# Optimization experiments

Measured on AMD Instinct MI355X. Metric: run time of the kernel, lower is better.

Reference implementation:

```python
import jax, jax.numpy as jnp
import numpy as np

NUM_HEADS = 16
CLAMP = 1e4


def setup_inputs() -> dict:
    key = jax.random.key(0)
    ks = jax.random.split(key, 8)
    B, Nq, Nkv, Cq, Ckv = 4, 2048, 2048, 1024, 768
    s_q = 1.0 / np.sqrt(Cq)
    s_kv = 1.0 / np.sqrt(Ckv)
    return {
        "query": jax.random.normal(ks[0], (B, Nq, Cq), jnp.float32),
        "key_value": jax.random.normal(ks[1], (B, Nkv, Ckv), jnp.float32),
        "Wq": jax.random.normal(ks[2], (Cq, Cq), jnp.float32) * s_q,
        "bq": jnp.zeros((Cq,), jnp.float32),
        "Wk": jax.random.normal(ks[3], (Ckv, Cq), jnp.float32) * s_kv,
        "bk": jnp.zeros((Cq,), jnp.float32),
        "Wv": jax.random.normal(ks[4], (Ckv, Cq), jnp.float32) * s_kv,
        "bv": jnp.zeros((Cq,), jnp.float32),
        "Wo": jax.random.normal(ks[5], (Cq, Cq), jnp.float32) * s_q,
        "bo": jnp.zeros((Cq,), jnp.float32),
    }


def reference(query, key_value, Wq, bq, Wk, bk, Wv, bv, Wo, bo):
    B, Nq, Cq = query.shape
    Nkv = key_value.shape[1]
    H = NUM_HEADS
    D = Cq // H
    scale = D ** (-0.5)

    # projections -> [B, H, N, D]
    q = (query @ Wq + bq).reshape(B, Nq, H, D).transpose(0, 2, 1, 3)
    k = (key_value @ Wk + bk).reshape(B, Nkv, H, D).transpose(0, 2, 1, 3)
    v = (key_value @ Wv + bv).reshape(B, Nkv, H, D).transpose(0, 2, 1, 3)

    # scores [B, H, Nq, Nkv] with clamp (mask=None path)
    attn = jnp.einsum("bhqd,bhkd->bhqk", q, k) * scale
    attn = jnp.clip(attn, -CLAMP, CLAMP)
    attn = jax.nn.softmax(attn, axis=-1)
    # NaN fallback: replace with uniform attention if any NaN present
    attn = jnp.where(jnp.any(jnp.isnan(attn)),
                     jnp.asarray(1.0 / Nkv, attn.dtype), attn)

    # weighted sum -> [B, Nq, Cq]
    x = jnp.einsum("bhqk,bhkd->bqhd", attn, v).reshape(B, Nq, Cq)
    return x @ Wo + bo
```

## Files before the change

### kernel.cpp

```cpp
#include <hip/hip_runtime.h>
#include <hip/hip_bf16.h>
#include <stdint.h>


typedef unsigned short u16;
typedef __attribute__((ext_vector_type(2))) float f32x2;
typedef __attribute__((ext_vector_type(4))) short bf16x4;
typedef __attribute__((ext_vector_type(8))) short bf16x8;
typedef __attribute__((ext_vector_type(4))) float f32x4;
typedef __attribute__((ext_vector_type(16))) float f32x16;

__device__ __forceinline__ u16 f2bf(float x) {
  union { float f; uint32_t u; } c; c.f = x;
  uint32_t r = c.u + 0x7fffu + ((c.u >> 16) & 1u);
  return (u16)(r >> 16);
}

__device__ __forceinline__ uint32_t pkbf(float a, float b) {
#if __has_builtin(__builtin_amdgcn_cvt_pk_bf16_f32)
  typedef __attribute__((ext_vector_type(2))) __bf16 bf2;
  bf2 r = __builtin_amdgcn_cvt_pk_bf16_f32(a, b);
  return __builtin_bit_cast(uint32_t, r);
#else
  return (uint32_t)f2bf(a) | ((uint32_t)f2bf(b) << 16);
#endif
}

__device__ __forceinline__ void gld16(const void* g, void* l) {
  __builtin_amdgcn_global_load_lds(
      (const __attribute__((address_space(1))) void*)g,
      (__attribute__((address_space(3))) void*)l, 16, 0, 0);
}

__device__ __forceinline__ void xcd_swz(int& bx, int& by) {
  int lin = by * 8 + bx;
  int x = lin & 7, y = lin >> 3;
  bx = y >> 3;
  by = (x << 3) | (y & 7);
}

__device__ __forceinline__ void cvt_body(const float* __restrict__ in,
                                         u16* __restrict__ out, int blk) {
  int i = (blk * 256 + threadIdx.x) * 8;
  float4 a = *(const float4*)(in + i);
  float4 b = *(const float4*)(in + i + 4);
  union { u16 u[8]; uint4 v; } o;
  o.u[0] = f2bf(a.x); o.u[1] = f2bf(a.y); o.u[2] = f2bf(a.z); o.u[3] = f2bf(a.w);
  o.u[4] = f2bf(b.x); o.u[5] = f2bf(b.y); o.u[6] = f2bf(b.z); o.u[7] = f2bf(b.w);
  *(uint4*)(out + i) = o.v;
}

__device__ __forceinline__ void transpose_body(const float* __restrict__ in,
                                               u16* __restrict__ out,
                                               int R, int C, int bx, int by) {
  __shared__ float tile[64][65];
  int c0 = bx * 64, r0 = by * 64;
  #pragma unroll
  for (int it = 0; it < 16; it++) {
    int idx = threadIdx.x + it * 256;
    int lr = idx >> 6, lc = idx & 63;
    tile[lr][lc] = in[(size_t)(r0 + lr) * C + c0 + lc];
  }
  __syncthreads();
  #pragma unroll
  for (int it = 0; it < 16; it++) {
    int idx = threadIdx.x + it * 256;
    int lc = idx >> 6, lr = idx & 63;
    out[(size_t)(c0 + lc) * R + r0 + lr] = f2bf(tile[lr][lc]);
  }
}

__global__ void prep_kernel(const float* __restrict__ query,
                            const float* __restrict__ key_value,
                            const float* __restrict__ Wq, const float* __restrict__ Wk,
                            const float* __restrict__ Wv, const float* __restrict__ Wo,
                            u16* qb, u16* kvb, u16* WqT, u16* WkT, u16* WvT, u16* WoT) {
  int blk = blockIdx.x;
  if (blk < 4096) { cvt_body(query, qb, blk); return; }
  if (blk < 7168) { cvt_body(key_value, kvb, blk - 4096); return; }
  if (blk < 7424) { int lo = blk - 7168; transpose_body(Wq, WqT, 1024, 1024, lo & 15, lo >> 4); return; }
  if (blk < 7616) { int lo = blk - 7424; transpose_body(Wk, WkT, 768, 1024, lo & 15, lo >> 4); return; }
  if (blk < 7808) { int lo = blk - 7616; transpose_body(Wv, WvT, 768, 1024, lo & 15, lo >> 4); return; }
  { int lo = blk - 7808; transpose_body(Wo, WoT, 1024, 1024, lo & 15, lo >> 4); return; }
}

template<bool SWAP>
__device__ __forceinline__ void gemm_kloop(const u16* __restrict__ A,
                                           const u16* __restrict__ BT,
                                           int K, char* smem, f32x4 (&acc)[4][4],
                                           int m0, int n0, int tid) {
  const u16* ap[4]; const u16* bp[4]; int ldA[4], ldB[4];
  #pragma unroll
  for (int it2 = 0; it2 < 4; it2++) {
    int s = it2 * 256 + tid;
    int row = s >> 3, cl = (s & 7) ^ (row & 7);
    ap[it2] = A + (size_t)(m0 + row) * K + cl * 8;
    bp[it2] = BT + (size_t)(n0 + row) * K + cl * 8;
    ldA[it2] = s * 16;
    ldB[it2] = 16384 + s * 16;
  }
  const int w = tid >> 6, l = tid & 63;
  const int lm = l & 15, lq = l >> 4;
  const int wr = w >> 1, wc = w & 1;
  int abase[4], bbase[4];
  #pragma unroll
  for (int i = 0; i < 4; i++) {
    int m = wr * 64 + i * 16 + lm;
    abase[i] = m * 128 + ((lq ^ (m & 7)) << 4);
    int n = wc * 64 + i * 16 + lm;
    bbase[i] = 16384 + n * 128 + ((lq ^ (n & 7)) << 4);
  }
  for (int k0 = 0; k0 < K; k0 += 64) {
    #pragma unroll
    for (int it2 = 0; it2 < 4; it2++) {
      gld16(ap[it2], smem + ldA[it2]);
      gld16(bp[it2], smem + ldB[it2]);
      ap[it2] += 64; bp[it2] += 64;
    }
    __syncthreads();
    #pragma unroll
    for (int kk = 0; kk < 2; kk++) {
      bf16x8 af[4], bf[4];
      #pragma unroll
      for (int i = 0; i < 4; i++)
        af[i] = *(const bf16x8*)(smem + (abase[i] ^ (kk << 6)));
      #pragma unroll
      for (int j = 0; j < 4; j++)
        bf[j] = *(const bf16x8*)(smem + (bbase[j] ^ (kk << 6)));
      #pragma unroll
      for (int i = 0; i < 4; i++)
        #pragma unroll
        for (int j = 0; j < 4; j++) {
          if (SWAP)
            acc[i][j] = __builtin_amdgcn_mfma_f32_16x16x32_bf16(bf[j], af[i], acc[i][j], 0, 0, 0);
          else
            acc[i][j] = __builtin_amdgcn_mfma_f32_16x16x32_bf16(af[i], bf[j], acc[i][j], 0, 0, 0);
        }
    }
    __syncthreads();
  }
}

__global__ __launch_bounds__(256, 3)
void gemm_qkv(const u16* __restrict__ qb, const u16* __restrict__ kvb,
              const u16* __restrict__ WqT, const u16* __restrict__ WkT,
              const u16* __restrict__ WvT,
              const float* __restrict__ bq, const float* __restrict__ bk,
              const float* __restrict__ bv,
              u16* __restrict__ Qb, u16* __restrict__ Kbf, u16* __restrict__ Vt,
              float qscale) {
  extern __shared__ __align__(16) char smem[];
  const int tid = threadIdx.x;
  const int w = tid >> 6, l = tid & 63;
  const int lm = l & 15, lq = l >> 4;
  int bxs = blockIdx.x, bys = blockIdx.y;
  xcd_swz(bxs, bys);
  const int m0 = bys * 128, n0 = bxs * 128;
  const int wr = w >> 1, wc = w & 1;
  const int z = blockIdx.z;
  f32x4 acc[4][4] = {};

  u16* etile = (u16*)(smem + w * 9216);
  const int xr = l >> 3, cc = (l & 7) ^ xr;

  if (z < 2) {
    const u16* A = (z == 0) ? qb : kvb;
    const u16* BT = (z == 0) ? WqT : WkT;
    const float* bias = (z == 0) ? bq : bk;
    u16* out = (z == 0) ? Qb : Kbf;
    const float scale = (z == 0) ? qscale : 1.0f;
    const int K = (z == 0) ? 1024 : 768;
    gemm_kloop<true>(A, BT, K, smem, acc, m0, n0, tid);
    #pragma unroll
    for (int j = 0; j < 4; j++) {
      float4 b4 = *(const float4*)&bias[n0 + wc * 64 + j * 16 + lq * 4];
      #pragma unroll
      for (int i = 0; i < 4; i++) {
        uint2 pkd;
        pkd.x = pkbf((acc[i][j][0] + b4.x) * scale, (acc[i][j][1] + b4.y) * scale);
        pkd.y = pkbf((acc[i][j][2] + b4.z) * scale, (acc[i][j][3] + b4.w) * scale);
        *(uint2*)&etile[(i * 16 + lm) * 72 + j * 16 + lq * 4] = pkd;
      }
    }
    u16* gbase = out + (size_t)(m0 + wr * 64) * 1024 + n0 + wc * 64;
    #pragma unroll
    for (int co = 0; co < 8; co++) {
      int ml = co * 8 + xr;
      uint4 d = *(const uint4*)&etile[ml * 72 + cc * 8];
      *(uint4*)&gbase[(size_t)ml * 1024 + cc * 8] = d;
    }
  } else {
    gemm_kloop<false>(kvb, WvT, 768, smem, acc, m0, n0, tid);
    #pragma unroll
    for (int j = 0; j < 4; j++) {
      float bi = bv[n0 + wc * 64 + j * 16 + lm];
      #pragma unroll
      for (int i = 0; i < 4; i++) {
        uint2 pkd;
        pkd.x = pkbf(acc[i][j][0] + bi, acc[i][j][1] + bi);
        pkd.y = pkbf(acc[i][j][2] + bi, acc[i][j][3] + bi);
        *(uint2*)&etile[(j * 16 + lm) * 72 + i * 16 + lq * 4] = pkd;
      }
    }
    const int bb = m0 >> 11, mloc = (m0 & 2047) + wr * 64;
    u16* gbase = Vt + ((size_t)bb * 1024 + n0 + wc * 64) * 2048 + mloc;
    const int kvA = (cc >> 1) * 16 + (cc & 1) * 4;
    #pragma unroll
    for (int co = 0; co < 8; co++) {
      int dl = co * 8 + xr;
      uint2 dA = *(const uint2*)&etile[dl * 72 + kvA];
      uint2 dB = *(const uint2*)&etile[dl * 72 + kvA + 8];
      uint4 d = {dA.x, dA.y, dB.x, dB.y};
      *(uint4*)&gbase[(size_t)dl * 2048 + cc * 8] = d;
    }
  }
}

__global__ __launch_bounds__(256, 3)
void gemm_o(const u16* __restrict__ A, const u16* __restrict__ BT,
            const float* __restrict__ bias, float* __restrict__ Cout) {
  __shared__ __align__(16) char smem[32768];
  const int tid = threadIdx.x;
  const int w = tid >> 6, l = tid & 63;
  const int lm = l & 15, lq = l >> 4;
  int bxs = blockIdx.x, bys = blockIdx.y;
  xcd_swz(bxs, bys);
  const int m0 = bys * 128, n0 = bxs * 128;
  const int wr = w >> 1, wc = w & 1;
  f32x4 acc[4][4] = {};
  gemm_kloop<false>(A, BT, 1024, smem, acc, m0, n0, tid);
  #pragma unroll
  for (int j = 0; j < 4; j++) {
    int gn = n0 + wc * 64 + j * 16 + lm;
    float bi = bias[gn];
    #pragma unroll
    for (int i = 0; i < 4; i++) {
      int gm = m0 + wr * 64 + i * 16 + lq * 4;
      #pragma unroll
      for (int r = 0; r < 4; r++)
        Cout[(size_t)(gm + r) * 1024 + gn] = acc[i][j][r] + bi;
    }
  }
}

__global__ __launch_bounds__(256, 2)
void attn_kernel(const u16* __restrict__ Q, const u16* __restrict__ Kb,
                 const u16* __restrict__ Vt, u16* __restrict__ X) {
  __shared__ __align__(16) char smem[32768];
  const int tid = threadIdx.x, w = tid >> 6, l = tid & 63;
  const int l31 = l & 31, h5 = l >> 5;
  const int bh = blockIdx.x, b = bh >> 4, h = bh & 15;
  const int q0 = blockIdx.y * 256 + w * 64;
  const int rx = l31 & 7;

  const u16* Kg = Kb + (size_t)b * 2048 * 1024 + h * 64;
  const u16* Vg = Vt + (size_t)bh * 64 * 2048;

  const u16 *kp0, *kp1, *vp0, *vp1;
  {
    int s = tid, r = s >> 3, c = (s & 7) ^ (r & 7);
    kp0 = Kg + (size_t)r * 1024 + c * 8;
    vp0 = Vg + (size_t)r * 2048 + c * 8;
    s = 256 + tid; r = s >> 3; c = (s & 7) ^ (r & 7);
    kp1 = Kg + (size_t)r * 1024 + c * 8;
    vp1 = Vg + (size_t)r * 2048 + c * 8;
  }
  const int kd0 = tid * 16, kd1 = (256 + tid) * 16;

  bf16x8 qfA[4], qfB[4];
  {
    const u16* qp = Q + ((size_t)(b * 2048 + q0 + l31)) * 1024 + h * 64 + h5 * 8;
    #pragma unroll
    for (int t = 0; t < 4; t++) qfA[t] = *(const bf16x8*)(qp + t * 16);
    qp += (size_t)32 * 1024;
    #pragma unroll
    for (int t = 0; t < 4; t++) qfB[t] = *(const bf16x8*)(qp + t * 16);
  }

  const int kvb2 = (l31 << 7) | ((rx ^ h5) << 4);
  const int vb2 = 16384 | (l31 << 7) | ((rx ^ h5) << 4);

  f32x16 xaccA[2] = {}, xaccB[2] = {};
  f32x2 lsA = {0.f, 0.f}, lsB = {0.f, 0.f};
  const f32x16 KZ = {};

  gld16(kp0, smem + kd0); gld16(kp1, smem + kd1);
  gld16(vp0, smem + 16384 + kd0); gld16(vp1, smem + 16384 + kd1);
  kp0 += 65536; kp1 += 65536; vp0 += 64; vp1 += 64;
  __syncthreads();

#define ATTN_STEP(CUR, DOPREF)                                                  \
  {                                                                             \
    if (DOPREF) {                                                               \
      const int nb = ((CUR) ^ 1) << 13;                                         \
      gld16(kp0, smem + nb + kd0); gld16(kp1, smem + nb + kd1);                 \
      gld16(vp0, smem + 16384 + nb + kd0); gld16(vp1, smem + 16384 + nb + kd1); \
      kp0 += 65536; kp1 += 65536; vp0 += 64; vp1 += 64;                         \
    }                                                                           \
    _Pragma("unroll")                                                           \
    for (int sub = 0; sub < 2; sub++) {                                         \
      const int km = ((CUR) << 13) | (sub << 12);                               \
      bf16x8 kf[4];                                                             \
      _Pragma("unroll")                                                         \
      for (int t = 0; t < 4; t++)                                               \
        kf[t] = *(const bf16x8*)(smem + (kvb2 ^ (km | (t << 5))));              \
      f32x16 st = __builtin_amdgcn_mfma_f32_32x32x16_bf16(kf[0], qfA[0], KZ, 0, 0, 0); \
      _Pragma("unroll")                                                         \
      for (int t = 1; t < 4; t++)                                               \
        st = __builtin_amdgcn_mfma_f32_32x32x16_bf16(kf[t], qfA[t], st, 0, 0, 0); \
      uint32_t pkA[8], pkB[8];                                                  \
      _Pragma("unroll")                                                         \
      for (int u = 0; u < 4; u++) {                                             \
        float p0 = __builtin_amdgcn_exp2f(st[4 * u + 0]);                       \
        float p1 = __builtin_amdgcn_exp2f(st[4 * u + 1]);                       \
        float p2 = __builtin_amdgcn_exp2f(st[4 * u + 2]);                       \
        float p3 = __builtin_amdgcn_exp2f(st[4 * u + 3]);                       \
        lsA += (f32x2){p0 + p2, p1 + p3};                                       \
        pkA[2 * u] = pkbf(p0, p1); pkA[2 * u + 1] = pkbf(p2, p3);               \
      }                                                                         \
      st = __builtin_amdgcn_mfma_f32_32x32x16_bf16(kf[0], qfB[0], KZ, 0, 0, 0); \
      _Pragma("unroll")                                                         \
      for (int t = 1; t < 4; t++)                                               \
        st = __builtin_amdgcn_mfma_f32_32x32x16_bf16(kf[t], qfB[t], st, 0, 0, 0); \
      _Pragma("unroll")                                                         \
      for (int u = 0; u < 4; u++) {                                             \
        float p0 = __builtin_amdgcn_exp2f(st[4 * u + 0]);                       \
        float p1 = __builtin_amdgcn_exp2f(st[4 * u + 1]);                       \
        float p2 = __builtin_amdgcn_exp2f(st[4 * u + 2]);                       \
        float p3 = __builtin_amdgcn_exp2f(st[4 * u + 3]);                       \
        lsB += (f32x2){p0 + p2, p1 + p3};                                       \
        pkB[2 * u] = pkbf(p0, p1); pkB[2 * u + 1] = pkbf(p2, p3);               \
      }                                                                         \
      _Pragma("unroll")                                                         \
      for (int c2 = 0; c2 < 2; c2++) {                                          \
        union { uint32_t d[4]; bf16x8 v; } pfA, pfB;                            \
        _Pragma("unroll")                                                       \
        for (int dd = 0; dd < 4; dd++) {                                        \
          pfA.d[dd] = pkA[4 * c2 + dd]; pfB.d[dd] = pkB[4 * c2 + dd];           \
        }                                                                       \
        const int vx = ((sub << 2) | (c2 << 1)) << 4;                           \
        _Pragma("unroll")                                                       \
        for (int dt = 0; dt < 2; dt++) {                                        \
          bf16x8 vf = *(const bf16x8*)(smem +                                   \
              (vb2 ^ (((CUR) << 13) | (dt << 12) | vx)));                       \
          xaccA[dt] = __builtin_amdgcn_mfma_f32_32x32x16_bf16(vf, pfA.v, xaccA[dt], 0, 0, 0); \
          xaccB[dt] = __builtin_amdgcn_mfma_f32_32x32x16_bf16(vf, pfB.v, xaccB[dt], 0, 0, 0); \
        }                                                                       \
      }                                                                         \
    }                                                                           \
    __syncthreads();                                                            \
  }

  for (int itp = 0; itp < 15; itp++) {
    ATTN_STEP(0, true)
    ATTN_STEP(1, true)
  }
  ATTN_STEP(0, true)
  ATTN_STEP(1, false)
#undef ATTN_STEP

  {
    float lsum = lsA[0] + lsA[1];
    const float inv = 1.0f / (lsum + __shfl_xor(lsum, 32));
    u16* xp = X + ((size_t)(b * 2048 + q0 + l31)) * 1024 + h * 64;
    #pragma unroll
    for (int dt = 0; dt < 2; dt++)
      #pragma unroll
      for (int g = 0; g < 4; g++) {
        const int d0 = dt * 32 + g * 8 + h5 * 4;
        uint2 o;
        o.x = pkbf(xaccA[dt][4 * g + 0] * inv, xaccA[dt][4 * g + 1] * inv);
        o.y = pkbf(xaccA[dt][4 * g + 2] * inv, xaccA[dt][4 * g + 3] * inv);
        *(uint2*)(xp + d0) = o;
      }
  }
  {
    float lsum = lsB[0] + lsB[1];
    const float inv = 1.0f / (lsum + __shfl_xor(lsum, 32));
    u16* xp = X + ((size_t)(b * 2048 + q0 + 32 + l31)) * 1024 + h * 64;
    #pragma unroll
    for (int dt = 0; dt < 2; dt++)
      #pragma unroll
      for (int g = 0; g < 4; g++) {
        const int d0 = dt * 32 + g * 8 + h5 * 4;
        uint2 o;
        o.x = pkbf(xaccB[dt][4 * g + 0] * inv, xaccB[dt][4 * g + 1] * inv);
        o.y = pkbf(xaccB[dt][4 * g + 2] * inv, xaccB[dt][4 * g + 3] * inv);
        *(uint2*)(xp + d0) = o;
      }
  }
}

extern "C" void kernel_launch(void* const* d_in, const int* in_sizes, int n_in,
                              void* d_out, int out_size, void* d_ws, size_t ws_size,
                              hipStream_t stream) {
  const float* query     = (const float*)d_in[0];
  const float* key_value = (const float*)d_in[1];
  const float* Wq = (const float*)d_in[2];
  const float* bq = (const float*)d_in[3];
  const float* Wk = (const float*)d_in[4];
  const float* bk = (const float*)d_in[5];
  const float* Wv = (const float*)d_in[6];
  const float* bv = (const float*)d_in[7];
  const float* Wo = (const float*)d_in[8];
  const float* bo = (const float*)d_in[9];
  float* out = (float*)d_out;

  char* ws = (char*)d_ws;
  size_t off = 0;
  auto alloc = [&](size_t bytes) -> void* {
    void* p = ws + off; off += (bytes + 255) & ~(size_t)255; return p;
  };
  u16* qb  = (u16*)alloc((size_t)8192 * 1024 * 2);
  u16* kvb = (u16*)alloc((size_t)8192 * 768 * 2);
  u16* WqT = (u16*)alloc((size_t)1024 * 1024 * 2);
  u16* WkT = (u16*)alloc((size_t)1024 * 768 * 2);
  u16* WvT = (u16*)alloc((size_t)1024 * 768 * 2);
  u16* WoT = (u16*)alloc((size_t)1024 * 1024 * 2);
  u16* Qb  = (u16*)alloc((size_t)8192 * 1024 * 2);
  u16* Kbf = (u16*)alloc((size_t)8192 * 1024 * 2);
  u16* Vt  = (u16*)alloc((size_t)8192 * 1024 * 2);
  u16* Xb  = (u16*)alloc((size_t)8192 * 1024 * 2);

  prep_kernel<<<8064, 256, 0, stream>>>(query, key_value, Wq, Wk, Wv, Wo,
                                        qb, kvb, WqT, WkT, WvT, WoT);

  const float qscale = 0.125f * 1.4426950408889634f;
  gemm_qkv<<<dim3(8, 64, 3), 256, 36864, stream>>>(qb, kvb, WqT, WkT, WvT,
                                                   bq, bk, bv, Qb, Kbf, Vt, qscale);

  attn_kernel<<<dim3(64, 8), 256, 0, stream>>>(Qb, Kbf, Vt, Xb);

  gemm_o<<<dim3(8, 64), 256, 0, stream>>>(Xb, WoT, bo, out);
}
```

Measured before the change: 279.3 us.

## Fuse K and V projections into one GEMM kernel sharing the A tile

Splits the merged QKV launch into a Q-only GEMM and a new K/V kernel. The new kernel loads each key_value tile once and multiplies it against both Wk and Wv, keeping two accumulator sets. This halves A-operand global and LDS traffic for the K and V projections. The cost is double the accumulator registers, occupancy lowered to 2 blocks per CU, 48KB of LDS, one extra kernel launch and a simpler non-pipelined k-loop.

```diff
diff --git a/kernel.cpp b/kernel.cpp
--- a/kernel.cpp
+++ b/kernel.cpp
@@ -157,62 +157,139 @@
   xcd_swz(bxs, bys);
   const int m0 = bys * 128, n0 = bxs * 128;
   const int wr = w >> 1, wc = w & 1;
-  const int z = blockIdx.z;
   f32x4 acc[4][4] = {};
 
   u16* etile = (u16*)(smem + w * 9216);
   const int xr = l >> 3, cc = (l & 7) ^ xr;
 
-  if (z < 2) {
-    const u16* A = (z == 0) ? qb : kvb;
-    const u16* BT = (z == 0) ? WqT : WkT;
-    const float* bias = (z == 0) ? bq : bk;
-    u16* out = (z == 0) ? Qb : Kbf;
-    const float scale = (z == 0) ? qscale : 1.0f;
-    const int K = (z == 0) ? 1024 : 768;
-    gemm_kloop<true>(A, BT, K, smem, acc, m0, n0, tid);
-    #pragma unroll
-    for (int j = 0; j < 4; j++) {
-      float4 b4 = *(const float4*)&bias[n0 + wc * 64 + j * 16 + lq * 4];
+  gemm_kloop<true>(qb, WqT, 1024, smem, acc, m0, n0, tid);
+  #pragma unroll
+  for (int j = 0; j < 4; j++) {
+    float4 b4 = *(const float4*)&bq[n0 + wc * 64 + j * 16 + lq * 4];
+    #pragma unroll
+    for (int i = 0; i < 4; i++) {
+      uint2 pkd;
+      pkd.x = pkbf((acc[i][j][0] + b4.x) * qscale, (acc[i][j][1] + b4.y) * qscale);
+      pkd.y = pkbf((acc[i][j][2] + b4.z) * qscale, (acc[i][j][3] + b4.w) * qscale);
+      *(uint2*)&etile[(i * 16 + lm) * 72 + j * 16 + lq * 4] = pkd;
+    }
+  }
+  u16* gbase = Qb + (size_t)(m0 + wr * 64) * 1024 + n0 + wc * 64;
+  #pragma unroll
+  for (int co = 0; co < 8; co++) {
+    int ml = co * 8 + xr;
+    uint4 d = *(const uint4*)&etile[ml * 72 + cc * 8];
+    *(uint4*)&gbase[(size_t)ml * 1024 + cc * 8] = d;
+  }
+}
+
+__global__ __launch_bounds__(256, 2)
+void gemm_kv(const u16* __restrict__ kvb,
+             const u16* __restrict__ WkT, const u16* __restrict__ WvT,
+             const float* __restrict__ bk, const float* __restrict__ bv,
+             u16* __restrict__ Kbf, u16* __restrict__ Vt) {
+  __shared__ __align__(16) char smem[49152];
+  const int tid = threadIdx.x;
+  const int w = tid >> 6, l = tid & 63;
+  const int lm = l & 15, lq = l >> 4;
+  int bxs = blockIdx.x, bys = blockIdx.y;
+  xcd_swz(bxs, bys);
+  const int m0 = bys * 128, n0 = bxs * 128;
+  const int wr = w >> 1, wc = w & 1;
+  f32x4 accK[4][4] = {}, accV[4][4] = {};
+
+  const u16* ap[4]; const u16* bkp[4]; const u16* bvp[4];
+  int sdst[4];
+  #pragma unroll
+  for (int it = 0; it < 4; it++) {
+    int s = it * 256 + tid;
+    int row = s >> 3, cl = (s & 7) ^ (row & 7);
+    ap[it]  = kvb + (size_t)(m0 + row) * 768 + cl * 8;
+    bkp[it] = WkT + (size_t)(n0 + row) * 768 + cl * 8;
+    bvp[it] = WvT + (size_t)(n0 + row) * 768 + cl * 8;
+    sdst[it] = s * 16;
+  }
+  int abase[4], bbase[4];
+  #pragma unroll
+  for (int i = 0; i < 4; i++) {
+    int m = wr * 64 + i * 16 + lm;
+    abase[i] = m * 128 + ((lq ^ (m & 7)) << 4);
+    int n = wc * 64 + i * 16 + lm;
+    bbase[i] = n * 128 + ((lq ^ (n & 7)) << 4);
+  }
+  for (int k0 = 0; k0 < 768; k0 += 64) {
+    #pragma unroll
+    for (int it = 0; it < 4; it++) {
+      gld16(ap[it],  smem + sdst[it]);
+      gld16(bkp[it], smem + 16384 + sdst[it]);
+      gld16(bvp[it], smem + 32768 + sdst[it]);
+      ap[it] += 64; bkp[it] += 64; bvp[it] += 64;
+    }
+    __syncthreads();
+    #pragma unroll
+    for (int kk = 0; kk < 2; kk++) {
+      bf16x8 af[4], bfk[4], bfv[4];
       #pragma unroll
       for (int i = 0; i < 4; i++) {
-        uint2 pkd;
-        pkd.x = pkbf((acc[i][j][0] + b4.x) * scale, (acc[i][j][1] + b4.y) * scale);
-        pkd.y = pkbf((acc[i][j][2] + b4.z) * scale, (acc[i][j][3] + b4.w) * scale);
-        *(uint2*)&etile[(i * 16 + lm) * 72 + j * 16 + lq * 4] = pkd;
+        af[i]  = *(const bf16x8*)(smem + (abase[i] ^ (kk << 6)));
+        bfk[i] = *(const bf16x8*)(smem + 16384 + (bbase[i] ^ (kk << 6)));
+        bfv[i] = *(const bf16x8*)(smem + 32768 + (bbase[i] ^ (kk << 6)));
       }
-    }
-    u16* gbase = out + (size_t)(m0 + wr * 64) * 1024 + n0 + wc * 64;
-    #pragma unroll
-    for (int co = 0; co < 8; co++) {
-      int ml = co * 8 + xr;
-      uint4 d = *(const uint4*)&etile[ml * 72 + cc * 8];
-      *(uint4*)&gbase[(size_t)ml * 1024 + cc * 8] = d;
-    }
-  } else {
-    gemm_kloop<false>(kvb, WvT, 768, smem, acc, m0, n0, tid);
-    #pragma unroll
-    for (int j = 0; j < 4; j++) {
-      float bi = bv[n0 + wc * 64 + j * 16 + lm];
-      #pragma unroll
-      for (int i = 0; i < 4; i++) {
-        uint2 pkd;
-        pkd.x = pkbf(acc[i][j][0] + bi, acc[i][j][1] + bi);
-        pkd.y = pkbf(acc[i][j][2] + bi, acc[i][j][3] + bi);
-        *(uint2*)&etile[(j * 16 + lm) * 72 + i * 16 + lq * 4] = pkd;
-      }
-    }
-    const int bb = m0 >> 11, mloc = (m0 & 2047) + wr * 64;
-    u16* gbase = Vt + ((size_t)bb * 1024 + n0 + wc * 64) * 2048 + mloc;
-    const int kvA = (cc >> 1) * 16 + (cc & 1) * 4;
-    #pragma unroll
-    for (int co = 0; co < 8; co++) {
-      int dl = co * 8 + xr;
-      uint2 dA = *(const uint2*)&etile[dl * 72 + kvA];
-      uint2 dB = *(const uint2*)&etile[dl * 72 + kvA + 8];
-      uint4 d = {dA.x, dA.y, dB.x, dB.y};
-      *(uint4*)&gbase[(size_t)dl * 2048 + cc * 8] = d;
-    }
+      #pragma unroll
+      for (int i = 0; i < 4; i++)
+        #pragma unroll
+        for (int j = 0; j < 4; j++) {
+          accK[i][j] = __builtin_amdgcn_mfma_f32_16x16x32_bf16(bfk[j], af[i], accK[i][j], 0, 0, 0);
+          accV[i][j] = __builtin_amdgcn_mfma_f32_16x16x32_bf16(af[i], bfv[j], accV[i][j], 0, 0, 0);
+        }
+    }
+    __syncthreads();
+  }
+
+  u16* etile = (u16*)(smem + w * 9216);
+  const int xr = l >> 3, cc = (l & 7) ^ xr;
+
+  #pragma unroll
+  for (int j = 0; j < 4; j++) {
+    float4 b4 = *(const float4*)&bk[n0 + wc * 64 + j * 16 + lq * 4];
+    #pragma unroll
+    for (int i = 0; i < 4; i++) {
+      uint2 pkd;
+      pkd.x = pkbf(accK[i][j][0] + b4.x, accK[i][j][1] + b4.y);
+      pkd.y = pkbf(accK[i][j][2] + b4.z, accK[i][j][3] + b4.w);
+      *(uint2*)&etile[(i * 16 + lm) * 72 + j * 16 + lq * 4] = pkd;
+    }
+  }
+  u16* gbase = Kbf + (size_t)(m0 + wr * 64) * 1024 + n0 + wc * 64;
+  #pragma unroll
+  for (int co = 0; co < 8; co++) {
+    int ml = co * 8 + xr;
+    uint4 d = *(const uint4*)&etile[ml * 72 + cc * 8];
+    *(uint4*)&gbase[(size_t)ml * 1024 + cc * 8] = d;
+  }
+  __syncthreads();
+
+  #pragma unroll
+  for (int j = 0; j < 4; j++) {
+    float bi = bv[n0 + wc * 64 + j * 16 + lm];
+    #pragma unroll
+    for (int i = 0; i < 4; i++) {
+      uint2 pkd;
+      pkd.x = pkbf(accV[i][j][0] + bi, accV[i][j][1] + bi);
+      pkd.y = pkbf(accV[i][j][2] + bi, accV[i][j][3] + bi);
+      *(uint2*)&etile[(j * 16 + lm) * 72 + i * 16 + lq * 4] = pkd;
+    }
+  }
+  const int bb = m0 >> 11, mloc = (m0 & 2047) + wr * 64;
+  u16* vbase = Vt + ((size_t)bb * 1024 + n0 + wc * 64) * 2048 + mloc;
+  const int kvA = (cc >> 1) * 16 + (cc & 1) * 4;
+  #pragma unroll
+  for (int co = 0; co < 8; co++) {
+    int dl = co * 8 + xr;
+    uint2 dA = *(const uint2*)&etile[dl * 72 + kvA];
+    uint2 dB = *(const uint2*)&etile[dl * 72 + kvA + 8];
+    uint4 d = {dA.x, dA.y, dB.x, dB.y};
+    *(uint4*)&vbase[(size_t)dl * 2048 + cc * 8] = d;
   }
 }
 
@@ -426,8 +503,9 @@
                                         qb, kvb, WqT, WkT, WvT, WoT);
 
   const float qscale = 0.125f * 1.4426950408889634f;
-  gemm_qkv<<<dim3(8, 64, 3), 256, 36864, stream>>>(qb, kvb, WqT, WkT, WvT,
+  gemm_qkv<<<dim3(8, 64, 1), 256, 36864, stream>>>(qb, kvb, WqT, WkT, WvT,
                                                    bq, bk, bv, Qb, Kbf, Vt, qscale);
+  gemm_kv<<<dim3(8, 64), 256, 0, stream>>>(kvb, WkT, WvT, bk, bv, Kbf, Vt);
 
   attn_kernel<<<dim3(64, 8), 256, 0, stream>>>(Qb, Kbf, Vt, Xb);
 
```

Result: faster. 273.5 us (-2.1%).
